# Kernel optimization log

Hardware: AMD Instinct MI355X
Metric: run time of the kernel (lower is better)

Reference implementation:

```python
import jax, jax.numpy as jnp
import numpy as np
import math

D_MODEL = 1024
D_ATTN = 128
D_MID = 128
L = 4096

def setup_inputs() -> dict:
    key = jax.random.key(0)
    ks = jax.random.split(key, 5)
    scale = 1.0 / math.sqrt(D_MODEL)
    return {
        "x": jax.random.normal(ks[0], (L, D_MODEL), jnp.float32),
        "z": jax.random.normal(ks[1], (L, D_MODEL), jnp.float32),
        "Wq": jax.random.normal(ks[2], (D_MODEL, D_ATTN), jnp.float32) * scale,
        "bq": jnp.zeros((D_ATTN,), jnp.float32),
        "Wk": jax.random.normal(ks[3], (D_MODEL, D_ATTN), jnp.float32) * scale,
        "bk": jnp.zeros((D_ATTN,), jnp.float32),
        "Wv": jax.random.normal(ks[4], (D_MODEL, D_MID), jnp.float32) * scale,
        "bv": jnp.zeros((D_MID,), jnp.float32),
    }

def reference(x, z, Wq, bq, Wk, bk, Wv, bv):
    # q: [L_x, d_attn], k: [L_z, d_attn], v: [L_z, d_mid]
    q = x @ Wq + bq
    k = z @ Wk + bk
    v = z @ Wv + bv
    inv_sqrt_d = 1.0 / math.sqrt(D_ATTN)
    s = (q @ k.T) * inv_sqrt_d            # [L_x, L_z]
    y = jax.nn.softmax(s, axis=-1) @ v    # [L_x, d_mid]
    return y
```

## Files before the change

### kernel.cpp

```cpp
#include <hip/hip_runtime.h>
#include <hip/hip_bf16.h>

typedef __attribute__((ext_vector_type(8))) short short8;
typedef __attribute__((ext_vector_type(4))) float f32x4;

#define L_SEQ 4096
#define DM    1024
#define DA    128
#define AZ    8

#define OFF_QB  786432
#define OFF_KF  1835008
#define OFF_VF  2883584
#define OFF_OA  4063232

__device__ __forceinline__ short f2bf(float f) {
    union { float f; unsigned u; } v; v.f = f;
    unsigned u = v.u;
    u += 0x7FFFu + ((u >> 16) & 1u);
    return (short)(u >> 16);
}

typedef const __attribute__((address_space(1))) void g_void_t;
typedef __attribute__((address_space(3))) void l_void_t;
__device__ __forceinline__ void g2lds16(const void* g, void* l) {
    __builtin_amdgcn_global_load_lds((g_void_t*)g, (l_void_t*)l, 16, 0, 0);
}

__global__ __launch_bounds__(256) void prep_w_kernel(
    const float* __restrict__ Wq, const float* __restrict__ Wk,
    const float* __restrict__ Wv, short8* __restrict__ WTf)
{
    const int m = blockIdx.y, kidx = blockIdx.x;
    const float* __restrict__ W = (m == 0) ? Wq : (m == 1) ? Wk : Wv;
    __shared__ __align__(16) float Ws[32 * 132];
    const int t = threadIdx.x;
#pragma unroll
    for (int i = 0; i < 4; i++) {
        const int u = i * 256 + t;
        const int kk = u >> 5, n4 = (u & 31) * 4;
        *(f32x4*)&Ws[kk * 132 + n4] = *(const f32x4*)&W[(size_t)(kidx * 32 + kk) * DA + n4];
    }
    __syncthreads();
#pragma unroll
    for (int i = 0; i < 2; i++) {
        const int u = i * 256 + t;
        const int nt = u >> 6, lane = u & 63, l16 = lane & 15, quad = lane >> 4;
        short8 fr;
#pragma unroll
        for (int j = 0; j < 8; j++)
            fr[j] = f2bf(Ws[(quad * 8 + j) * 132 + nt * 16 + l16]);
        WTf[((size_t)(m * 32 + kidx) * 8 + nt) * 64 + lane] = fr;
    }
}

__global__ __launch_bounds__(256, 1) void qkv_kernel(
    const float* __restrict__ x, const float* __restrict__ z,
    const char* __restrict__ WTraw,
    const float* __restrict__ bq, const float* __restrict__ bk,
    const float* __restrict__ bv,
    short* __restrict__ qb, short8* __restrict__ kf, short8* __restrict__ vf)
{
    __shared__ __align__(16) char smem[2][32768];

    const int t = threadIdx.x;
    const int wave = t >> 6, lane = t & 63;
    const int l16 = lane & 15, quad = lane >> 4;
    const int mtile = wave >> 1, nhalf = wave & 1;
    const int isKV = blockIdx.y;
    const int m1 = isKV ? 1 : 0;
    const int row0 = blockIdx.x * 32;
    const int nbytes = isKV ? 32768 : 16384;

    const float* __restrict__ Am = isKV ? z : x;
    const float* ap = Am + (size_t)(row0 + mtile * 16 + l16) * DM + quad * 8;

    f32x4 acc1[4], acc2[4];
#pragma unroll
    for (int i = 0; i < 4; i++) {
        acc1[i] = (f32x4){0.f, 0.f, 0.f, 0.f};
        acc2[i] = (f32x4){0.f, 0.f, 0.f, 0.f};
    }

    auto stage = [&](int it2, int b) {
        const char* base1 = WTraw + (size_t)(m1 * 32 + it2 * 2) * 8192;
        const char* base2 = WTraw + (size_t)(2 * 32 + it2 * 2) * 8192;
#pragma unroll
        for (int i = 0; i < 8; i++) {
            const int off = i * 4096 + wave * 1024;
            if (off < nbytes) {
                const char* src = (off < 16384) ? (base1 + off) : (base2 + (off - 16384));
                g2lds16(src + lane * 16, &smem[b][off]);
            }
        }
    };

    f32x4 cur[4], nxt[4];
#pragma unroll
    for (int j = 0; j < 2; j++) {
        cur[j * 2]     = *(const f32x4*)(ap + j * 32);
        cur[j * 2 + 1] = *(const f32x4*)(ap + j * 32 + 4);
        nxt[j * 2]     = *(const f32x4*)(ap + 64 + j * 32);
        nxt[j * 2 + 1] = *(const f32x4*)(ap + 64 + j * 32 + 4);
    }

    stage(0, 0);
    __syncthreads();

#pragma unroll 1
    for (int it = 0; it < 16; it++) {
        const int b = it & 1;
        if (it + 1 < 16) stage(it + 1, b ^ 1);

        const int ipf = (it + 2 < 16) ? it + 2 : it;
        f32x4 fut[4];
#pragma unroll
        for (int j = 0; j < 2; j++) {
            fut[j * 2]     = *(const f32x4*)(ap + ipf * 64 + j * 32);
            fut[j * 2 + 1] = *(const f32x4*)(ap + ipf * 64 + j * 32 + 4);
        }

#pragma unroll
        for (int ss = 0; ss < 2; ss++) {
            short8 afr;
#pragma unroll
            for (int j = 0; j < 4; j++) {
                afr[j]     = f2bf(cur[ss * 2][j]);
                afr[4 + j] = f2bf(cur[ss * 2 + 1][j]);
            }
#pragma unroll
            for (int ntl = 0; ntl < 4; ntl++) {
                short8 bfr = *(const short8*)&smem[b][ss * 8192 + ((nhalf * 4 + ntl) * 64 + lane) * 16];
                acc1[ntl] = __builtin_amdgcn_mfma_f32_16x16x32_bf16(afr, bfr, acc1[ntl], 0, 0, 0);
            }
            if (isKV) {
#pragma unroll
                for (int ntl = 0; ntl < 4; ntl++) {
                    short8 bfr = *(const short8*)&smem[b][16384 + ss * 8192 + ((nhalf * 4 + ntl) * 64 + lane) * 16];
                    acc2[ntl] = __builtin_amdgcn_mfma_f32_16x16x32_bf16(afr, bfr, acc2[ntl], 0, 0, 0);
                }
            }
        }
        __syncthreads();
#pragma unroll
        for (int j = 0; j < 4; j++) { cur[j] = nxt[j]; nxt[j] = fut[j]; }
    }

    if (!isKV) {
#pragma unroll
        for (int ntl = 0; ntl < 4; ntl++) {
            const int col = nhalf * 64 + ntl * 16 + l16;
            const float bb = bq[col];
#pragma unroll
            for (int r = 0; r < 4; r++)
                qb[(size_t)(row0 + mtile * 16 + quad * 4 + r) * DA + col] =
                    f2bf(acc1[ntl][r] + bb);
        }
        return;
    }

    short* kT = (short*)&smem[0][0];
    short* vT = (short*)&smem[0][16384];
#pragma unroll
    for (int ntl = 0; ntl < 4; ntl++) {
        const int col = nhalf * 64 + ntl * 16 + l16;
        const float bbk = bk[col], bbv = bv[col];
#pragma unroll
        for (int r = 0; r < 4; r++) {
            const int rl = mtile * 16 + quad * 4 + r;
            kT[rl * 132 + col] = f2bf(acc1[ntl][r] + bbk);
            vT[rl * 132 + col] = f2bf(acc2[ntl][r] + bbv);
        }
    }
    __syncthreads();

    const int kg = blockIdx.x;
#pragma unroll
    for (int i = 0; i < 2; i++) {
        const int f = i * 256 + t;
        const int ks = f >> 7, nth = (f >> 6) & 1, ln = f & 63;
        const int lf = ln & 15, qf = ln >> 4;
        short8 fr;
#pragma unroll
        for (int j = 0; j < 8; j++)
            fr[j] = kT[(nth * 16 + lf) * 132 + ks * 32 + qf * 8 + j];
        kf[((size_t)(kg * 4 + ks) * 2 + nth) * 64 + ln] = fr;
    }
#pragma unroll
    for (int i = 0; i < 3; i++) {
        const int f = i * 256 + t;
        if (f < 576) {
            const int nt = f >> 6, ln = f & 63;
            const int lf = ln & 15, qf = ln >> 4;
            short8 fr;
            if (nt < 8) {
#pragma unroll
                for (int j = 0; j < 8; j++)
                    fr[j] = vT[(qf * 8 + j) * 132 + nt * 16 + lf];
            } else {
                const short one = (short)0x3F80;
#pragma unroll
                for (int j = 0; j < 8; j++) fr[j] = (lf == 0) ? one : (short)0;
            }
            vf[((size_t)kg * 9 + nt) * 64 + ln] = fr;
        }
    }
}

__global__ __launch_bounds__(256, 2) void attn_kernel(
    const short* __restrict__ qb, const char* __restrict__ kfg,
    const char* __restrict__ vfg, float* __restrict__ OA,
    float* __restrict__ lA)
{
    __shared__ __align__(16) char kv[2][17408];
    __shared__ __align__(16) short Ps[4][16 * 40];

    const int t    = threadIdx.x;
    const int wave = t >> 6;
    const int lane = t & 63;
    const int l16  = lane & 15;
    const int quad = lane >> 4;
    const int qr0  = blockIdx.x * 64;
    const int g0   = blockIdx.y * 16;

    auto stage = [&](int g, int b) {
        const char* kb_ = kfg + (size_t)(g0 + g) * 8192;
        const char* vb_ = vfg + (size_t)(g0 + g) * 9216;
#pragma unroll
        for (int i = 0; i < 5; i++) {
            const int off = i * 4096 + wave * 1024;
            if (off < 17408) {
                const char* src = (off < 8192) ? (kb_ + off) : (vb_ + (off - 8192));
                g2lds16(src + lane * 16, &kv[b][off]);
            }
        }
    };

    stage(0, 0);

    short8 af[4];
    const short* qrow = qb + (size_t)(qr0 + wave * 16 + l16) * DA + quad * 8;
#pragma unroll
    for (int ks = 0; ks < 4; ks++)
        af[ks] = *(const short8*)(qrow + ks * 32);

    f32x4 O[9];
#pragma unroll
    for (int i = 0; i < 9; i++) O[i] = (f32x4){0.f, 0.f, 0.f, 0.f};

    const float C = 0.08838834764831845f;
    short* P = &Ps[wave][0];

    __syncthreads();

#pragma unroll 1
    for (int g = 0; g < 16; g++) {
        const int b = g & 1;
        if (g + 1 < 16) stage(g + 1, b ^ 1);

        const char* kb_ = &kv[b][0];
        const char* vb_ = &kv[b][8192];

        f32x4 s0[2];
#pragma unroll
        for (int nh = 0; nh < 2; nh++) s0[nh] = (f32x4){0.f, 0.f, 0.f, 0.f};
#pragma unroll
        for (int nh = 0; nh < 2; nh++)
#pragma unroll
            for (int ks = 0; ks < 4; ks++) {
                short8 bfr = *(const short8*)(kb_ + ((ks * 2 + nh) * 64 + lane) * 16);
                s0[nh] = __builtin_amdgcn_mfma_f32_16x16x32_bf16(af[ks], bfr, s0[nh], 0, 0, 0);
            }

#pragma unroll
        for (int nh = 0; nh < 2; nh++)
#pragma unroll
            for (int r = 0; r < 4; r++)
                P[(quad * 4 + r) * 40 + nh * 16 + l16] = f2bf(__expf(s0[nh][r] * C));
        asm volatile("" ::: "memory");
        __builtin_amdgcn_s_waitcnt(0xc07f);
        asm volatile("" ::: "memory");

        short8 a2 = *(const short8*)&P[l16 * 40 + quad * 8];
#pragma unroll
        for (int nt = 0; nt < 9; nt++) {
            short8 b2 = *(const short8*)(vb_ + (nt * 64 + lane) * 16);
            O[nt] = __builtin_amdgcn_mfma_f32_16x16x32_bf16(a2, b2, O[nt], 0, 0, 0);
        }
        __syncthreads();
    }

    const int rw = qr0 + wave * 16;
    float* Ob = OA + (size_t)blockIdx.y * L_SEQ * DA;
#pragma unroll
    for (int nt = 0; nt < 8; nt++)
#pragma unroll
        for (int r = 0; r < 4; r++)
            Ob[(size_t)(rw + quad * 4 + r) * DA + nt * 16 + l16] = O[nt][r];
    if (l16 == 0) {
        float* lb = lA + (size_t)blockIdx.y * L_SEQ;
#pragma unroll
        for (int r = 0; r < 4; r++)
            lb[rw + quad * 4 + r] = O[8][r];
    }
}

__global__ __launch_bounds__(256) void merge_kernel(
    const float* __restrict__ OA, const float* __restrict__ lA,
    float* __restrict__ out)
{
    const int t = threadIdx.x;
    const int row = blockIdx.x * 16 + (t >> 4);
    const int cg = (t & 15) * 8;

    f32x4 a0 = (f32x4){0.f, 0.f, 0.f, 0.f};
    f32x4 a1 = (f32x4){0.f, 0.f, 0.f, 0.f};
    float lsum = 0.f;
#pragma unroll
    for (int zz = 0; zz < AZ; zz++) {
        const float* p = &OA[((size_t)zz * L_SEQ + row) * DA + cg];
        a0 = a0 + *(const f32x4*)p;
        a1 = a1 + *(const f32x4*)(p + 4);
        lsum += lA[(size_t)zz * L_SEQ + row];
    }
    const float inv = 1.f / lsum;
    f32x4* dst = (f32x4*)&out[(size_t)row * DA + cg];
    dst[0] = a0 * inv;
    dst[1] = a1 * inv;
}

extern "C" void kernel_launch(void* const* d_in, const int* in_sizes, int n_in,
                              void* d_out, int out_size, void* d_ws, size_t ws_size,
                              hipStream_t stream) {
    (void)in_sizes; (void)n_in; (void)out_size; (void)ws_size;
    const float* x  = (const float*)d_in[0];
    const float* z  = (const float*)d_in[1];
    const float* Wq = (const float*)d_in[2];
    const float* bq = (const float*)d_in[3];
    const float* Wk = (const float*)d_in[4];
    const float* bk = (const float*)d_in[5];
    const float* Wv = (const float*)d_in[6];
    const float* bv = (const float*)d_in[7];
    float* out = (float*)d_out;

    short8* WTf = (short8*)d_ws;
    short*  qb  = (short*)((char*)d_ws + OFF_QB);
    short8* kf  = (short8*)((char*)d_ws + OFF_KF);
    short8* vf  = (short8*)((char*)d_ws + OFF_VF);
    float*  OA  = (float*)((char*)d_ws + OFF_OA);
    float*  lA  = (float*)((char*)d_ws + OFF_OA + (size_t)AZ * L_SEQ * DA * 4);

    prep_w_kernel<<<dim3(32, 3), 256, 0, stream>>>(Wq, Wk, Wv, WTf);
    qkv_kernel<<<dim3(128, 2), 256, 0, stream>>>(x, z, (const char*)WTf,
                                                 bq, bk, bv, qb, kf, vf);
    attn_kernel<<<dim3(64, AZ), 256, 0, stream>>>(qb, (const char*)kf,
                                                  (const char*)vf, OA, lA);
    merge_kernel<<<256, 256, 0, stream>>>(OA, lA, out);
}
```

Before: 130.7 us.

## Split QKV projection over K into partials and double attention KV splits

The QKV projection kernel now splits the 1024-wide reduction into four slices across a third grid dimension and writes fp32 partial sums. A new finalize kernel adds the partials and bias, converts to bf16 and performs the K/V fragment relayout. The attention split count doubles from 8 to 16, so each block handles fewer key groups. Together these raise parallelism on the GPU, at the cost of extra fp32 partial traffic, an additional launch, and a larger merge workload.

```diff
diff --git a/kernel.cpp b/kernel.cpp
--- a/kernel.cpp
+++ b/kernel.cpp
@@ -7,12 +7,15 @@
 #define L_SEQ 4096
 #define DM    1024
 #define DA    128
-#define AZ    8
-
-#define OFF_QB  786432
-#define OFF_KF  1835008
-#define OFF_VF  2883584
-#define OFF_OA  4063232
+#define PS    4
+#define AZ    16
+
+#define OFF_QB   786432
+#define OFF_KF   1835008
+#define OFF_VF   2883584
+#define OFF_OA   4063232
+#define OFF_LA   (OFF_OA + (size_t)AZ * L_SEQ * DA * 4)
+#define OFF_PART (OFF_LA + (size_t)AZ * L_SEQ * 4 + 1048576)
 
 __device__ __forceinline__ short f2bf(float f) {
     union { float f; unsigned u; } v; v.f = f;
@@ -54,26 +57,25 @@
     }
 }
 
-__global__ __launch_bounds__(256, 1) void qkv_kernel(
+__global__ __launch_bounds__(256, 2) void qkvp_kernel(
     const float* __restrict__ x, const float* __restrict__ z,
-    const char* __restrict__ WTraw,
-    const float* __restrict__ bq, const float* __restrict__ bk,
-    const float* __restrict__ bv,
-    short* __restrict__ qb, short8* __restrict__ kf, short8* __restrict__ vf)
-{
-    __shared__ __align__(16) char smem[2][32768];
+    const char* __restrict__ WTraw, float* __restrict__ part)
+{
+    __shared__ __align__(16) char smem[2][16384];
 
     const int t = threadIdx.x;
     const int wave = t >> 6, lane = t & 63;
     const int l16 = lane & 15, quad = lane >> 4;
     const int mtile = wave >> 1, nhalf = wave & 1;
     const int isKV = blockIdx.y;
+    const int s = blockIdx.z;
     const int m1 = isKV ? 1 : 0;
     const int row0 = blockIdx.x * 32;
-    const int nbytes = isKV ? 32768 : 16384;
+    const int nbytes = isKV ? 16384 : 8192;
+    const int ks0 = s * 8;
 
     const float* __restrict__ Am = isKV ? z : x;
-    const float* ap = Am + (size_t)(row0 + mtile * 16 + l16) * DM + quad * 8;
+    const float* ap = Am + (size_t)(row0 + mtile * 16 + l16) * DM + s * 256 + quad * 8;
 
     f32x4 acc1[4], acc2[4];
 #pragma unroll
@@ -82,127 +84,141 @@
         acc2[i] = (f32x4){0.f, 0.f, 0.f, 0.f};
     }
 
-    auto stage = [&](int it2, int b) {
-        const char* base1 = WTraw + (size_t)(m1 * 32 + it2 * 2) * 8192;
-        const char* base2 = WTraw + (size_t)(2 * 32 + it2 * 2) * 8192;
-#pragma unroll
-        for (int i = 0; i < 8; i++) {
+    auto stage = [&](int kidx, int b) {
+        const char* base1 = WTraw + (size_t)(m1 * 32 + kidx) * 8192;
+        const char* base2 = WTraw + (size_t)(2 * 32 + kidx) * 8192;
+#pragma unroll
+        for (int i = 0; i < 4; i++) {
             const int off = i * 4096 + wave * 1024;
             if (off < nbytes) {
-                const char* src = (off < 16384) ? (base1 + off) : (base2 + (off - 16384));
+                const char* src = (off < 8192) ? (base1 + off) : (base2 + (off - 8192));
                 g2lds16(src + lane * 16, &smem[b][off]);
             }
         }
     };
 
-    f32x4 cur[4], nxt[4];
-#pragma unroll
-    for (int j = 0; j < 2; j++) {
-        cur[j * 2]     = *(const f32x4*)(ap + j * 32);
-        cur[j * 2 + 1] = *(const f32x4*)(ap + j * 32 + 4);
-        nxt[j * 2]     = *(const f32x4*)(ap + 64 + j * 32);
-        nxt[j * 2 + 1] = *(const f32x4*)(ap + 64 + j * 32 + 4);
-    }
-
-    stage(0, 0);
+    f32x4 c0 = *(const f32x4*)ap,        c1 = *(const f32x4*)(ap + 4);
+    f32x4 d0 = *(const f32x4*)(ap + 32), d1 = *(const f32x4*)(ap + 36);
+
+    stage(ks0, 0);
     __syncthreads();
 
 #pragma unroll 1
-    for (int it = 0; it < 16; it++) {
-        const int b = it & 1;
-        if (it + 1 < 16) stage(it + 1, b ^ 1);
-
-        const int ipf = (it + 2 < 16) ? it + 2 : it;
-        f32x4 fut[4];
-#pragma unroll
-        for (int j = 0; j < 2; j++) {
-            fut[j * 2]     = *(const f32x4*)(ap + ipf * 64 + j * 32);
-            fut[j * 2 + 1] = *(const f32x4*)(ap + ipf * 64 + j * 32 + 4);
-        }
-
-#pragma unroll
-        for (int ss = 0; ss < 2; ss++) {
-            short8 afr;
-#pragma unroll
-            for (int j = 0; j < 4; j++) {
-                afr[j]     = f2bf(cur[ss * 2][j]);
-                afr[4 + j] = f2bf(cur[ss * 2 + 1][j]);
-            }
+    for (int ks = 0; ks < 8; ks++) {
+        const int b = ks & 1;
+        if (ks + 1 < 8) stage(ks0 + ks + 1, b ^ 1);
+
+        const int kpf = (ks + 2 < 8) ? ks + 2 : ks;
+        f32x4 e0 = *(const f32x4*)(ap + kpf * 32);
+        f32x4 e1 = *(const f32x4*)(ap + kpf * 32 + 4);
+
+        short8 afr;
+#pragma unroll
+        for (int j = 0; j < 4; j++) {
+            afr[j]     = f2bf(c0[j]);
+            afr[4 + j] = f2bf(c1[j]);
+        }
+
+#pragma unroll
+        for (int ntl = 0; ntl < 4; ntl++) {
+            short8 bfr = *(const short8*)&smem[b][((nhalf * 4 + ntl) * 64 + lane) * 16];
+            acc1[ntl] = __builtin_amdgcn_mfma_f32_16x16x32_bf16(afr, bfr, acc1[ntl], 0, 0, 0);
+        }
+        if (isKV) {
 #pragma unroll
             for (int ntl = 0; ntl < 4; ntl++) {
-                short8 bfr = *(const short8*)&smem[b][ss * 8192 + ((nhalf * 4 + ntl) * 64 + lane) * 16];
-                acc1[ntl] = __builtin_amdgcn_mfma_f32_16x16x32_bf16(afr, bfr, acc1[ntl], 0, 0, 0);
-            }
-            if (isKV) {
-#pragma unroll
-                for (int ntl = 0; ntl < 4; ntl++) {
-                    short8 bfr = *(const short8*)&smem[b][16384 + ss * 8192 + ((nhalf * 4 + ntl) * 64 + lane) * 16];
-                    acc2[ntl] = __builtin_amdgcn_mfma_f32_16x16x32_bf16(afr, bfr, acc2[ntl], 0, 0, 0);
-                }
+                short8 bfr = *(const short8*)&smem[b][8192 + ((nhalf * 4 + ntl) * 64 + lane) * 16];
+                acc2[ntl] = __builtin_amdgcn_mfma_f32_16x16x32_bf16(afr, bfr, acc2[ntl], 0, 0, 0);
             }
         }
         __syncthreads();
-#pragma unroll
-        for (int j = 0; j < 4; j++) { cur[j] = nxt[j]; nxt[j] = fut[j]; }
-    }
-
-    if (!isKV) {
+        c0 = d0; c1 = d1; d0 = e0; d1 = e1;
+    }
+
+    float* p1 = part + (size_t)(s * 3 + m1) * L_SEQ * DA;
+#pragma unroll
+    for (int ntl = 0; ntl < 4; ntl++) {
+        const int col = nhalf * 64 + ntl * 16 + l16;
+#pragma unroll
+        for (int r = 0; r < 4; r++)
+            p1[(size_t)(row0 + mtile * 16 + quad * 4 + r) * DA + col] = acc1[ntl][r];
+    }
+    if (isKV) {
+        float* p2 = part + (size_t)(s * 3 + 2) * L_SEQ * DA;
 #pragma unroll
         for (int ntl = 0; ntl < 4; ntl++) {
             const int col = nhalf * 64 + ntl * 16 + l16;
-            const float bb = bq[col];
 #pragma unroll
             for (int r = 0; r < 4; r++)
-                qb[(size_t)(row0 + mtile * 16 + quad * 4 + r) * DA + col] =
-                    f2bf(acc1[ntl][r] + bb);
-        }
-        return;
-    }
-
-    short* kT = (short*)&smem[0][0];
-    short* vT = (short*)&smem[0][16384];
-#pragma unroll
-    for (int ntl = 0; ntl < 4; ntl++) {
-        const int col = nhalf * 64 + ntl * 16 + l16;
-        const float bbk = bk[col], bbv = bv[col];
-#pragma unroll
-        for (int r = 0; r < 4; r++) {
-            const int rl = mtile * 16 + quad * 4 + r;
-            kT[rl * 132 + col] = f2bf(acc1[ntl][r] + bbk);
-            vT[rl * 132 + col] = f2bf(acc2[ntl][r] + bbv);
+                p2[(size_t)(row0 + mtile * 16 + quad * 4 + r) * DA + col] = acc2[ntl][r];
+        }
+    }
+}
+
+__global__ __launch_bounds__(256) void finalize_kernel(
+    const float* __restrict__ part,
+    const float* __restrict__ bq, const float* __restrict__ bk,
+    const float* __restrict__ bv,
+    short* __restrict__ qb, short8* __restrict__ kf, short8* __restrict__ vf)
+{
+    const int t = threadIdx.x;
+    const int row0 = blockIdx.x * 32;
+    __shared__ short Ts[DA * 33];
+
+#pragma unroll 1
+    for (int m = 0; m < 3; m++) {
+        const float* __restrict__ bias = (m == 0) ? bq : (m == 1) ? bk : bv;
+#pragma unroll
+        for (int i = 0; i < 2; i++) {
+            const int u = i * 256 + t;
+            const int r = u >> 4, cg8 = u & 15;
+            const int R = row0 + r, c0 = cg8 * 8;
+            float vsum[8];
+#pragma unroll
+            for (int j = 0; j < 8; j++) vsum[j] = bias[c0 + j];
+            for (int s = 0; s < PS; s++) {
+                const float* p = &part[((size_t)(s * 3 + m) * L_SEQ + R) * DA + c0];
+                f32x4 f0 = *(const f32x4*)p;
+                f32x4 f1 = *(const f32x4*)(p + 4);
+#pragma unroll
+                for (int j = 0; j < 4; j++) { vsum[j] += f0[j]; vsum[4 + j] += f1[j]; }
+            }
+            short8 o;
+#pragma unroll
+            for (int j = 0; j < 8; j++) o[j] = f2bf(vsum[j]);
+
+            if (m == 0) {
+                *(short8*)&qb[(size_t)R * DA + c0] = o;
+            } else if (m == 1) {
+                const int kg = R >> 5, nth = (R >> 4) & 1, l16 = R & 15;
+                const int ks = cg8 >> 2, quad = cg8 & 3;
+                kf[((size_t)(kg * 4 + ks) * 2 + nth) * 64 + quad * 16 + l16] = o;
+            } else {
+#pragma unroll
+                for (int j = 0; j < 8; j++) Ts[(c0 + j) * 33 + r] = o[j];
+            }
         }
     }
     __syncthreads();
 
-    const int kg = blockIdx.x;
-#pragma unroll
-    for (int i = 0; i < 2; i++) {
-        const int f = i * 256 + t;
-        const int ks = f >> 7, nth = (f >> 6) & 1, ln = f & 63;
-        const int lf = ln & 15, qf = ln >> 4;
-        short8 fr;
-#pragma unroll
-        for (int j = 0; j < 8; j++)
-            fr[j] = kT[(nth * 16 + lf) * 132 + ks * 32 + qf * 8 + j];
-        kf[((size_t)(kg * 4 + ks) * 2 + nth) * 64 + ln] = fr;
-    }
+    const int vg = blockIdx.x;
 #pragma unroll
     for (int i = 0; i < 3; i++) {
-        const int f = i * 256 + t;
-        if (f < 576) {
-            const int nt = f >> 6, ln = f & 63;
+        const int u = i * 256 + t;
+        if (u < 576) {
+            const int nt = u >> 6, ln = u & 63;
             const int lf = ln & 15, qf = ln >> 4;
             short8 fr;
             if (nt < 8) {
-#pragma unroll
-                for (int j = 0; j < 8; j++)
-                    fr[j] = vT[(qf * 8 + j) * 132 + nt * 16 + lf];
+                const int col = nt * 16 + lf;
+#pragma unroll
+                for (int j = 0; j < 8; j++) fr[j] = Ts[col * 33 + qf * 8 + j];
             } else {
                 const short one = (short)0x3F80;
 #pragma unroll
                 for (int j = 0; j < 8; j++) fr[j] = (lf == 0) ? one : (short)0;
             }
-            vf[((size_t)kg * 9 + nt) * 64 + ln] = fr;
+            vf[((size_t)vg * 9 + nt) * 64 + ln] = fr;
         }
     }
 }
@@ -221,7 +237,7 @@
     const int l16  = lane & 15;
     const int quad = lane >> 4;
     const int qr0  = blockIdx.x * 64;
-    const int g0   = blockIdx.y * 16;
+    const int g0   = blockIdx.y * 8;
 
     auto stage = [&](int g, int b) {
         const char* kb_ = kfg + (size_t)(g0 + g) * 8192;
@@ -254,9 +270,9 @@
     __syncthreads();
 
 #pragma unroll 1
-    for (int g = 0; g < 16; g++) {
+    for (int g = 0; g < 8; g++) {
         const int b = g & 1;
-        if (g + 1 < 16) stage(g + 1, b ^ 1);
+        if (g + 1 < 8) stage(g + 1, b ^ 1);
 
         const char* kb_ = &kv[b][0];
         const char* vb_ = &kv[b][8192];
@@ -343,16 +359,17 @@
     const float* bv = (const float*)d_in[7];
     float* out = (float*)d_out;
 
-    short8* WTf = (short8*)d_ws;
-    short*  qb  = (short*)((char*)d_ws + OFF_QB);
-    short8* kf  = (short8*)((char*)d_ws + OFF_KF);
-    short8* vf  = (short8*)((char*)d_ws + OFF_VF);
-    float*  OA  = (float*)((char*)d_ws + OFF_OA);
-    float*  lA  = (float*)((char*)d_ws + OFF_OA + (size_t)AZ * L_SEQ * DA * 4);
+    short8* WTf  = (short8*)d_ws;
+    short*  qb   = (short*)((char*)d_ws + OFF_QB);
+    short8* kf   = (short8*)((char*)d_ws + OFF_KF);
+    short8* vf   = (short8*)((char*)d_ws + OFF_VF);
+    float*  OA   = (float*)((char*)d_ws + OFF_OA);
+    float*  lA   = (float*)((char*)d_ws + OFF_LA);
+    float*  part = (float*)((char*)d_ws + OFF_PART);
 
     prep_w_kernel<<<dim3(32, 3), 256, 0, stream>>>(Wq, Wk, Wv, WTf);
-    qkv_kernel<<<dim3(128, 2), 256, 0, stream>>>(x, z, (const char*)WTf,
-                                                 bq, bk, bv, qb, kf, vf);
+    qkvp_kernel<<<dim3(128, 2, PS), 256, 0, stream>>>(x, z, (const char*)WTf, part);
+    finalize_kernel<<<128, 256, 0, stream>>>(part, bq, bk, bv, qb, kf, vf);
     attn_kernel<<<dim3(64, AZ), 256, 0, stream>>>(qb, (const char*)kf,
                                                   (const char*)vf, OA, lA);
     merge_kernel<<<256, 256, 0, stream>>>(OA, lA, out);
```

Result: no change. 131.7 us (+0.7%).

## Halve qkv row tile and double attention key splits for more parallelism

Applied to the files above, without the earlier changes.

The QKV projection kernel now processes 16 rows per block, with each wave owning 32 output columns. This doubles the grid to 512 blocks, halves shared memory and allows two blocks per CU. The K/V fragment repacking is split across pairs of blocks, and the block-wide barrier before it becomes a wave-local LDS waitcnt. The attention kernel's split-K factor goes from 8 to 16, which doubles its grid and the partial outputs the merge kernel must combine. The aim is to fill the 256 CUs better, at the cost of more merge traffic and more workspace.

```diff
diff --git a/kernel.cpp b/kernel.cpp
--- a/kernel.cpp
+++ b/kernel.cpp
@@ -7,12 +7,13 @@
 #define L_SEQ 4096
 #define DM    1024
 #define DA    128
-#define AZ    8
-
-#define OFF_QB  786432
-#define OFF_KF  1835008
-#define OFF_VF  2883584
-#define OFF_OA  4063232
+#define AZ    16
+
+#define OFF_QB   786432
+#define OFF_KF   1835008
+#define OFF_VF   2883584
+#define OFF_OA   4063232
+#define OFF_LA   (OFF_OA + (size_t)AZ * L_SEQ * DA * 4)
 
 __device__ __forceinline__ short f2bf(float f) {
     union { float f; unsigned u; } v; v.f = f;
@@ -54,155 +55,137 @@
     }
 }
 
-__global__ __launch_bounds__(256, 1) void qkv_kernel(
+__global__ __launch_bounds__(256, 2) void qkv_kernel(
     const float* __restrict__ x, const float* __restrict__ z,
     const char* __restrict__ WTraw,
     const float* __restrict__ bq, const float* __restrict__ bk,
     const float* __restrict__ bv,
     short* __restrict__ qb, short8* __restrict__ kf, short8* __restrict__ vf)
 {
-    __shared__ __align__(16) char smem[2][32768];
+    __shared__ __align__(16) char smem[2][16384];
 
     const int t = threadIdx.x;
-    const int wave = t >> 6, lane = t & 63;
+    const int w = t >> 6, lane = t & 63;
     const int l16 = lane & 15, quad = lane >> 4;
-    const int mtile = wave >> 1, nhalf = wave & 1;
     const int isKV = blockIdx.y;
-    const int m1 = isKV ? 1 : 0;
-    const int row0 = blockIdx.x * 32;
-    const int nbytes = isKV ? 32768 : 16384;
+    const int row0 = blockIdx.x * 16;
+    const int nbytes = isKV ? 16384 : 8192;
 
     const float* __restrict__ Am = isKV ? z : x;
-    const float* ap = Am + (size_t)(row0 + mtile * 16 + l16) * DM + quad * 8;
-
-    f32x4 acc1[4], acc2[4];
-#pragma unroll
-    for (int i = 0; i < 4; i++) {
+    const float* ap = Am + (size_t)(row0 + l16) * DM + quad * 8;
+
+    f32x4 acc1[2], acc2[2];
+#pragma unroll
+    for (int i = 0; i < 2; i++) {
         acc1[i] = (f32x4){0.f, 0.f, 0.f, 0.f};
         acc2[i] = (f32x4){0.f, 0.f, 0.f, 0.f};
     }
 
-    auto stage = [&](int it2, int b) {
-        const char* base1 = WTraw + (size_t)(m1 * 32 + it2 * 2) * 8192;
-        const char* base2 = WTraw + (size_t)(2 * 32 + it2 * 2) * 8192;
-#pragma unroll
-        for (int i = 0; i < 8; i++) {
-            const int off = i * 4096 + wave * 1024;
+    auto stage = [&](int kidx, int b) {
+        const char* base1 = WTraw + (size_t)(isKV * 32 + kidx) * 8192;
+        const char* base2 = WTraw + (size_t)(64 + kidx) * 8192;
+#pragma unroll
+        for (int i = 0; i < 4; i++) {
+            const int off = i * 4096 + w * 1024;
             if (off < nbytes) {
-                const char* src = (off < 16384) ? (base1 + off) : (base2 + (off - 16384));
+                const char* src = (off < 8192) ? (base1 + off) : (base2 + (off - 8192));
                 g2lds16(src + lane * 16, &smem[b][off]);
             }
         }
     };
 
-    f32x4 cur[4], nxt[4];
-#pragma unroll
-    for (int j = 0; j < 2; j++) {
-        cur[j * 2]     = *(const f32x4*)(ap + j * 32);
-        cur[j * 2 + 1] = *(const f32x4*)(ap + j * 32 + 4);
-        nxt[j * 2]     = *(const f32x4*)(ap + 64 + j * 32);
-        nxt[j * 2 + 1] = *(const f32x4*)(ap + 64 + j * 32 + 4);
-    }
+    f32x4 c0 = *(const f32x4*)ap,        c1 = *(const f32x4*)(ap + 4);
+    f32x4 d0 = *(const f32x4*)(ap + 32), d1 = *(const f32x4*)(ap + 36);
 
     stage(0, 0);
     __syncthreads();
 
 #pragma unroll 1
-    for (int it = 0; it < 16; it++) {
-        const int b = it & 1;
-        if (it + 1 < 16) stage(it + 1, b ^ 1);
-
-        const int ipf = (it + 2 < 16) ? it + 2 : it;
-        f32x4 fut[4];
-#pragma unroll
-        for (int j = 0; j < 2; j++) {
-            fut[j * 2]     = *(const f32x4*)(ap + ipf * 64 + j * 32);
-            fut[j * 2 + 1] = *(const f32x4*)(ap + ipf * 64 + j * 32 + 4);
-        }
-
-#pragma unroll
-        for (int ss = 0; ss < 2; ss++) {
-            short8 afr;
-#pragma unroll
-            for (int j = 0; j < 4; j++) {
-                afr[j]     = f2bf(cur[ss * 2][j]);
-                afr[4 + j] = f2bf(cur[ss * 2 + 1][j]);
+    for (int ks = 0; ks < 32; ks++) {
+        const int b = ks & 1;
+        if (ks + 1 < 32) stage(ks + 1, b ^ 1);
+
+        const int kpf = (ks + 2 < 32) ? ks + 2 : ks;
+        f32x4 e0 = *(const f32x4*)(ap + kpf * 32);
+        f32x4 e1 = *(const f32x4*)(ap + kpf * 32 + 4);
+
+        short8 afr;
+#pragma unroll
+        for (int j = 0; j < 4; j++) {
+            afr[j]     = f2bf(c0[j]);
+            afr[4 + j] = f2bf(c1[j]);
+        }
+
+#pragma unroll
+        for (int ntl = 0; ntl < 2; ntl++) {
+            short8 bfr = *(const short8*)&smem[b][((w * 2 + ntl) * 64 + lane) * 16];
+            acc1[ntl] = __builtin_amdgcn_mfma_f32_16x16x32_bf16(afr, bfr, acc1[ntl], 0, 0, 0);
+        }
+        if (isKV) {
+#pragma unroll
+            for (int ntl = 0; ntl < 2; ntl++) {
+                short8 bfr = *(const short8*)&smem[b][8192 + ((w * 2 + ntl) * 64 + lane) * 16];
+                acc2[ntl] = __builtin_amdgcn_mfma_f32_16x16x32_bf16(afr, bfr, acc2[ntl], 0, 0, 0);
             }
-#pragma unroll
-            for (int ntl = 0; ntl < 4; ntl++) {
-                short8 bfr = *(const short8*)&smem[b][ss * 8192 + ((nhalf * 4 + ntl) * 64 + lane) * 16];
-                acc1[ntl] = __builtin_amdgcn_mfma_f32_16x16x32_bf16(afr, bfr, acc1[ntl], 0, 0, 0);
-            }
-            if (isKV) {
-#pragma unroll
-                for (int ntl = 0; ntl < 4; ntl++) {
-                    short8 bfr = *(const short8*)&smem[b][16384 + ss * 8192 + ((nhalf * 4 + ntl) * 64 + lane) * 16];
-                    acc2[ntl] = __builtin_amdgcn_mfma_f32_16x16x32_bf16(afr, bfr, acc2[ntl], 0, 0, 0);
-                }
-            }
         }
         __syncthreads();
-#pragma unroll
-        for (int j = 0; j < 4; j++) { cur[j] = nxt[j]; nxt[j] = fut[j]; }
+        c0 = d0; c1 = d1; d0 = e0; d1 = e1;
     }
 
     if (!isKV) {
 #pragma unroll
-        for (int ntl = 0; ntl < 4; ntl++) {
-            const int col = nhalf * 64 + ntl * 16 + l16;
+        for (int ntl = 0; ntl < 2; ntl++) {
+            const int col = w * 32 + ntl * 16 + l16;
             const float bb = bq[col];
 #pragma unroll
             for (int r = 0; r < 4; r++)
-                qb[(size_t)(row0 + mtile * 16 + quad * 4 + r) * DA + col] =
-                    f2bf(acc1[ntl][r] + bb);
+                qb[(size_t)(row0 + quad * 4 + r) * DA + col] = f2bf(acc1[ntl][r] + bb);
         }
         return;
     }
 
     short* kT = (short*)&smem[0][0];
-    short* vT = (short*)&smem[0][16384];
-#pragma unroll
-    for (int ntl = 0; ntl < 4; ntl++) {
-        const int col = nhalf * 64 + ntl * 16 + l16;
+    short* vT = kT + 16 * 132;
+#pragma unroll
+    for (int ntl = 0; ntl < 2; ntl++) {
+        const int col = w * 32 + ntl * 16 + l16;
         const float bbk = bk[col], bbv = bv[col];
 #pragma unroll
         for (int r = 0; r < 4; r++) {
-            const int rl = mtile * 16 + quad * 4 + r;
+            const int rl = quad * 4 + r;
             kT[rl * 132 + col] = f2bf(acc1[ntl][r] + bbk);
             vT[rl * 132 + col] = f2bf(acc2[ntl][r] + bbv);
         }
     }
-    __syncthreads();
-
-    const int kg = blockIdx.x;
-#pragma unroll
-    for (int i = 0; i < 2; i++) {
-        const int f = i * 256 + t;
-        const int ks = f >> 7, nth = (f >> 6) & 1, ln = f & 63;
-        const int lf = ln & 15, qf = ln >> 4;
+    asm volatile("" ::: "memory");
+    __builtin_amdgcn_s_waitcnt(0xc07f);
+    asm volatile("" ::: "memory");
+
+    const int kg = blockIdx.x >> 1, nth = blockIdx.x & 1;
+    {
         short8 fr;
 #pragma unroll
         for (int j = 0; j < 8; j++)
-            fr[j] = kT[(nth * 16 + lf) * 132 + ks * 32 + qf * 8 + j];
-        kf[((size_t)(kg * 4 + ks) * 2 + nth) * 64 + ln] = fr;
-    }
-#pragma unroll
-    for (int i = 0; i < 3; i++) {
-        const int f = i * 256 + t;
-        if (f < 576) {
-            const int nt = f >> 6, ln = f & 63;
-            const int lf = ln & 15, qf = ln >> 4;
+            fr[j] = kT[l16 * 132 + w * 32 + quad * 8 + j];
+        kf[((size_t)(kg * 4 + w) * 2 + nth) * 64 + lane] = fr;
+    }
+    if ((quad >> 1) == nth) {
+        const int lr0 = (quad - 2 * nth) * 8;
+#pragma unroll
+        for (int ntl = 0; ntl < 2; ntl++) {
+            const int nt = w * 2 + ntl;
             short8 fr;
-            if (nt < 8) {
-#pragma unroll
-                for (int j = 0; j < 8; j++)
-                    fr[j] = vT[(qf * 8 + j) * 132 + nt * 16 + lf];
-            } else {
-                const short one = (short)0x3F80;
-#pragma unroll
-                for (int j = 0; j < 8; j++) fr[j] = (lf == 0) ? one : (short)0;
-            }
-            vf[((size_t)kg * 9 + nt) * 64 + ln] = fr;
+#pragma unroll
+            for (int j = 0; j < 8; j++)
+                fr[j] = vT[(lr0 + j) * 132 + nt * 16 + l16];
+            vf[((size_t)kg * 9 + nt) * 64 + lane] = fr;
+        }
+        if (w == 3) {
+            const short one = (short)0x3F80;
+            short8 fr;
+#pragma unroll
+            for (int j = 0; j < 8; j++) fr[j] = (l16 == 0) ? one : (short)0;
+            vf[((size_t)kg * 9 + 8) * 64 + lane] = fr;
         }
     }
 }
@@ -221,7 +204,7 @@
     const int l16  = lane & 15;
     const int quad = lane >> 4;
     const int qr0  = blockIdx.x * 64;
-    const int g0   = blockIdx.y * 16;
+    const int g0   = blockIdx.y * 8;
 
     auto stage = [&](int g, int b) {
         const char* kb_ = kfg + (size_t)(g0 + g) * 8192;
@@ -254,9 +237,9 @@
     __syncthreads();
 
 #pragma unroll 1
-    for (int g = 0; g < 16; g++) {
+    for (int g = 0; g < 8; g++) {
         const int b = g & 1;
-        if (g + 1 < 16) stage(g + 1, b ^ 1);
+        if (g + 1 < 8) stage(g + 1, b ^ 1);
 
         const char* kb_ = &kv[b][0];
         const char* vb_ = &kv[b][8192];
@@ -348,10 +331,10 @@
     short8* kf  = (short8*)((char*)d_ws + OFF_KF);
     short8* vf  = (short8*)((char*)d_ws + OFF_VF);
     float*  OA  = (float*)((char*)d_ws + OFF_OA);
-    float*  lA  = (float*)((char*)d_ws + OFF_OA + (size_t)AZ * L_SEQ * DA * 4);
+    float*  lA  = (float*)((char*)d_ws + OFF_LA);
 
     prep_w_kernel<<<dim3(32, 3), 256, 0, stream>>>(Wq, Wk, Wv, WTf);
-    qkv_kernel<<<dim3(128, 2), 256, 0, stream>>>(x, z, (const char*)WTf,
+    qkv_kernel<<<dim3(256, 2), 256, 0, stream>>>(x, z, (const char*)WTf,
                                                  bq, bk, bv, qb, kf, vf);
     attn_kernel<<<dim3(64, AZ), 256, 0, stream>>>(qb, (const char*)kf,
                                                   (const char*)vf, OA, lA);
```

Result: slower. 135.1 us (+3.4%).
